# Kernel optimization log

Hardware: AMD Instinct MI355X
Metric: run time of the kernel (lower is better)

## Reference

```python
import jax, jax.numpy as jnp
import numpy as np

D_MODEL = 1024
N_HEADS = 16
HEAD_DIM = 64
N_KV_HEADS = 4
D_FF = 4096
LN_EPS = 1e-5


def setup_inputs() -> dict:
    key = jax.random.key(0)
    ks = jax.random.split(key, 10)
    s = lambda fan_in: 1.0 / np.sqrt(fan_in)
    return {
        "x": jax.random.normal(ks[0], (2, 2048, D_MODEL), dtype=jnp.float32),
        "ln_w": jnp.ones((D_MODEL,), dtype=jnp.float32),
        "ln_b": jnp.zeros((D_MODEL,), dtype=jnp.float32),
        # Linear weights stored as (in, out): y = x @ W
        "wq": jax.random.normal(ks[1], (D_MODEL, N_HEADS * HEAD_DIM), dtype=jnp.float32) * s(D_MODEL),
        "wk": jax.random.normal(ks[2], (D_MODEL, N_KV_HEADS * HEAD_DIM), dtype=jnp.float32) * s(D_MODEL),
        "wv": jax.random.normal(ks[3], (D_MODEL, N_KV_HEADS * HEAD_DIM), dtype=jnp.float32) * s(D_MODEL),
        "wo": jax.random.normal(ks[4], (N_HEADS * HEAD_DIM, D_MODEL), dtype=jnp.float32) * s(N_HEADS * HEAD_DIM),
        "w_gate": jax.random.normal(ks[5], (D_MODEL, D_FF), dtype=jnp.float32) * s(D_MODEL),
        "w_up": jax.random.normal(ks[6], (D_MODEL, D_FF), dtype=jnp.float32) * s(D_MODEL),
        "w_down": jax.random.normal(ks[7], (D_FF, D_MODEL), dtype=jnp.float32) * s(D_FF),
    }


def _layernorm(x, w, b):
    mu = jnp.mean(x, axis=-1, keepdims=True)
    var = jnp.var(x, axis=-1, keepdims=True)
    return (x - mu) * jax.lax.rsqrt(var + LN_EPS) * w + b


def _attention(normed, wq, wk, wv, wo):
    B, S, _ = normed.shape
    h, kh, hd = N_HEADS, N_KV_HEADS, HEAD_DIM
    groups = h // kh
    scale = 1.0 / np.sqrt(hd)
    q = (normed @ wq).reshape(B, S, h, hd).transpose(0, 2, 1, 3)   # [B,h,S,hd]
    k = (normed @ wk).reshape(B, S, kh, hd).transpose(0, 2, 1, 3)  # [B,kh,S,hd]
    v = (normed @ wv).reshape(B, S, kh, hd).transpose(0, 2, 1, 3)
    if groups != 1:
        # matches torch repeat_interleave along head dim
        k = jnp.repeat(k, groups, axis=1)
        v = jnp.repeat(v, groups, axis=1)
    scores = jnp.einsum("bhqd,bhkd->bhqk", q, k) * scale
    causal = jnp.tril(jnp.ones((S, S), dtype=bool))
    scores = jnp.where(causal, scores, -jnp.inf)
    attn = jax.nn.softmax(scores, axis=-1)
    out = jnp.einsum("bhqk,bhkd->bhqd", attn, v)
    out = out.transpose(0, 2, 1, 3).reshape(B, S, h * hd)
    return out @ wo


def _ffn(normed, w_gate, w_up, w_down):
    return (jax.nn.silu(normed @ w_gate) * (normed @ w_up)) @ w_down


def reference(x, ln_w, ln_b, wq, wk, wv, wo, w_gate, w_up, w_down):
    normed = _layernorm(x, ln_w, ln_b)
    attn_out = _attention(normed, wq, wk, wv, wo)
    ffn_out = _ffn(normed, w_gate, w_up, w_down)
    return x + attn_out + ffn_out
```

## Files before the change

### kernel.cpp

```cpp
#include <hip/hip_runtime.h>
#include <cstdint>

typedef __bf16 bf16x8 __attribute__((ext_vector_type(8)));
typedef float f32x4 __attribute__((ext_vector_type(4)));
typedef float f32x16 __attribute__((ext_vector_type(16)));
typedef unsigned short u16;

#define MFMA16(a, b, c) __builtin_amdgcn_mfma_f32_16x16x32_bf16((a), (b), (c), 0, 0, 0)
#define MFMA32(a, b, c) __builtin_amdgcn_mfma_f32_32x32x16_bf16((a), (b), (c), 0, 0, 0)

#define GLLDS(gp, lp) __builtin_amdgcn_global_load_lds( \
    (const __attribute__((address_space(1))) uint32_t*)(gp), \
    (__attribute__((address_space(3))) uint32_t*)(lp), 16, 0, 0)

__device__ __forceinline__ u16 f2bf(float f) {
    union { float f; uint32_t u; } v; v.f = f;
    uint32_t u = v.u;
    u += 0x7FFFu + ((u >> 16) & 1u);
    return (u16)(u >> 16);
}
__device__ __forceinline__ float bf2f(u16 h) {
    union { uint32_t u; float f; } v; v.u = ((uint32_t)h) << 16;
    return v.f;
}

__global__ __launch_bounds__(256) void prep_kernel(
    const float* __restrict__ wq, const float* __restrict__ wk,
    const float* __restrict__ wv, const float* __restrict__ wo,
    const float* __restrict__ wg, const float* __restrict__ wu,
    const float* __restrict__ wd,
    const float* __restrict__ x, const float* __restrict__ ln_w,
    const float* __restrict__ ln_b,
    u16* __restrict__ QKVT, u16* __restrict__ WOT, u16* __restrict__ WGT,
    u16* __restrict__ WUT, u16* __restrict__ WDT, u16* __restrict__ NORMED) {
    const int bid = blockIdx.x;
    const int tid = threadIdx.x;

    if (bid < 14848) {
        const float* in; u16* out; int R, C, gx; int t = bid;
        if (t < 1024)              { in = wq; out = QKVT;                         R = 1024; C = 1024; gx = 32; }
        else if ((t -= 1024) < 256)  { in = wk; out = QKVT + (size_t)1024 * 1024; R = 1024; C = 256;  gx = 8; }
        else if ((t -= 256) < 256)   { in = wv; out = QKVT + (size_t)1280 * 1024; R = 1024; C = 256;  gx = 8; }
        else if ((t -= 256) < 1024)  { in = wo; out = WOT;                        R = 1024; C = 1024; gx = 32; }
        else if ((t -= 1024) < 4096) { in = wg; out = WGT;                        R = 1024; C = 4096; gx = 128; }
        else if ((t -= 4096) < 4096) { in = wu; out = WUT;                        R = 1024; C = 4096; gx = 128; }
        else          { t -= 4096;     in = wd; out = WDT;                        R = 4096; C = 1024; gx = 32; }
        const int bx = t % gx, by = t / gx;
        __shared__ float tile[32][33];
        const int c0 = bx * 32, r0 = by * 32;
        const int tx = tid & 31, ty = tid >> 5;
#pragma unroll
        for (int i = ty; i < 32; i += 8)
            tile[i][tx] = in[(size_t)(r0 + i) * C + c0 + tx];
        __syncthreads();
#pragma unroll
        for (int i = ty; i < 32; i += 8)
            out[(size_t)(c0 + i) * R + r0 + tx] = f2bf(tile[tx][i]);
    } else {
        const int row = bid - 14848;
        float4 v = ((const float4*)(x + (size_t)row * 1024))[tid];
        float s = v.x + v.y + v.z + v.w;
        float s2 = v.x * v.x + v.y * v.y + v.z * v.z + v.w * v.w;
#pragma unroll
        for (int off = 1; off < 64; off <<= 1) {
            s += __shfl_xor(s, off);
            s2 += __shfl_xor(s2, off);
        }
        __shared__ float rs[4], rs2[4];
        const int wv4i = tid >> 6;
        if ((tid & 63) == 0) { rs[wv4i] = s; rs2[wv4i] = s2; }
        __syncthreads();
        s = rs[0] + rs[1] + rs[2] + rs[3];
        s2 = rs2[0] + rs2[1] + rs2[2] + rs2[3];
        float mu = s * (1.0f / 1024.0f);
        float var = s2 * (1.0f / 1024.0f) - mu * mu;
        float inv = rsqrtf(var + 1e-5f);
        float4 wv4 = ((const float4*)ln_w)[tid];
        float4 bv4 = ((const float4*)ln_b)[tid];
        ushort4 o;
        o.x = f2bf((v.x - mu) * inv * wv4.x + bv4.x);
        o.y = f2bf((v.y - mu) * inv * wv4.y + bv4.y);
        o.z = f2bf((v.z - mu) * inv * wv4.z + bv4.z);
        o.w = f2bf((v.w - mu) * inv * wv4.w + bv4.w);
        *(ushort4*)(NORMED + (size_t)row * 1024 + tid * 4) = o;
    }
}

__global__ __launch_bounds__(256) void transpose_v(const u16* __restrict__ in, u16* __restrict__ out,
                                                   int in_stride) {
    __shared__ u16 tile[32][33];
    int b = blockIdx.z;
    int c0 = blockIdx.x * 32, s0 = blockIdx.y * 32;
    int tx = threadIdx.x & 31, ty = threadIdx.x >> 5;
#pragma unroll
    for (int i = ty; i < 32; i += 8)
        tile[i][tx] = in[(size_t)(b * 2048 + s0 + i) * in_stride + c0 + tx];
    __syncthreads();
#pragma unroll
    for (int i = ty; i < 32; i += 8)
        out[(size_t)b * 256 * 2048 + (size_t)(c0 + i) * 2048 + s0 + tx] = tile[tx][i];
}

__global__ __launch_bounds__(256) void gemm_bt64(const u16* __restrict__ A, const u16* __restrict__ Bt,
                                                 void* __restrict__ Cv,
                                                 int N, int K, int mode) {
    __shared__ __align__(16) u16 As[128 * 64];
    __shared__ __align__(16) u16 Bs[64 * 64];
    const int tid = threadIdx.x, lane = tid & 63, wv = tid >> 6;
    const int row0 = blockIdx.x * 128, col0 = blockIdx.y * 64;
    const int wr = (wv >> 1) * 64, wc = (wv & 1) * 32;
    const int fr = lane & 15, fg = lane >> 4;
    const int lr8 = lane >> 3;
    const int lc8s = ((lane & 7) ^ lr8) * 8;

    f32x4 acc[4][2];
#pragma unroll
    for (int i = 0; i < 4; ++i)
#pragma unroll
        for (int j = 0; j < 2; ++j) acc[i][j] = (f32x4){0.f, 0.f, 0.f, 0.f};

    const u16* ga = A + (size_t)(row0 + 32 * wv + lr8) * K + lc8s;
    const u16* gb = Bt + (size_t)(col0 + 16 * wv + lr8) * K + lc8s;
    u16* la = As + wv * 2048;
    u16* lb = Bs + wv * 1024;
    const int f7 = fr & 7;

    for (int k0 = 0; k0 < K; k0 += 64) {
        __syncthreads();
        GLLDS(ga + k0, la);
        GLLDS(ga + (size_t)8 * K + k0, la + 512);
        GLLDS(ga + (size_t)16 * K + k0, la + 1024);
        GLLDS(ga + (size_t)24 * K + k0, la + 1536);
        GLLDS(gb + k0, lb);
        GLLDS(gb + (size_t)8 * K + k0, lb + 512);
        __syncthreads();
#pragma unroll
        for (int kk = 0; kk < 2; ++kk) {
            bf16x8 af[4], bfr[2];
#pragma unroll
            for (int i = 0; i < 4; ++i)
                af[i] = *(const bf16x8*)(As + (wr + i * 16 + fr) * 64 + (((kk * 4 + fg) ^ f7) * 8));
#pragma unroll
            for (int j = 0; j < 2; ++j)
                bfr[j] = *(const bf16x8*)(Bs + (wc + j * 16 + fr) * 64 + (((kk * 4 + fg) ^ f7) * 8));
#pragma unroll
            for (int i = 0; i < 4; ++i)
#pragma unroll
                for (int j = 0; j < 2; ++j)
                    acc[i][j] = MFMA16(af[i], bfr[j], acc[i][j]);
        }
    }

    if (mode == 0) {
        u16* C = (u16*)Cv;
#pragma unroll
        for (int i = 0; i < 4; ++i)
#pragma unroll
            for (int j = 0; j < 2; ++j)
#pragma unroll
                for (int r = 0; r < 4; ++r) {
                    int row = row0 + wr + i * 16 + fg * 4 + r;
                    int col = col0 + wc + j * 16 + fr;
                    C[(size_t)row * N + col] = f2bf(acc[i][j][r]);
                }
    } else {
        float* C = (float*)Cv;
#pragma unroll
        for (int i = 0; i < 4; ++i)
#pragma unroll
            for (int j = 0; j < 2; ++j)
#pragma unroll
                for (int r = 0; r < 4; ++r) {
                    int row = row0 + wr + i * 16 + fg * 4 + r;
                    int col = col0 + wc + j * 16 + fr;
                    C[(size_t)row * N + col] = acc[i][j][r];
                }
    }
}

__global__ __launch_bounds__(256) void gemm_out_fused(const u16* __restrict__ A1,
                                                      const u16* __restrict__ B1t,
                                                      const u16* __restrict__ A2,
                                                      const u16* __restrict__ B2t,
                                                      const float* __restrict__ xres,
                                                      float* __restrict__ C) {
    __shared__ __align__(16) u16 As[128 * 64];
    __shared__ __align__(16) u16 Bs[64 * 64];
    const int tid = threadIdx.x, lane = tid & 63, wv = tid >> 6;
    const int row0 = blockIdx.x * 128, col0 = blockIdx.y * 64;
    const int wr = (wv >> 1) * 64, wc = (wv & 1) * 32;
    const int fr = lane & 15, fg = lane >> 4;
    const int lr8 = lane >> 3;
    const int lc8s = ((lane & 7) ^ lr8) * 8;
    const int f7 = fr & 7;

    f32x4 acc[4][2];
#pragma unroll
    for (int i = 0; i < 4; ++i)
#pragma unroll
        for (int j = 0; j < 2; ++j) acc[i][j] = (f32x4){0.f, 0.f, 0.f, 0.f};

    const int rowA = row0 + 32 * wv + lr8;
    const int rowB = col0 + 16 * wv + lr8;
    u16* la = As + wv * 2048;
    u16* lb = Bs + wv * 1024;

    for (int t = 0; t < 80; ++t) {
        const u16* ga;
        const u16* gb;
        size_t sa, sb;
        if (t < 16) {
            const int ko = t * 64;
            ga = A1 + (size_t)rowA * 1024 + ko + lc8s; sa = 1024;
            gb = B1t + (size_t)rowB * 1024 + ko + lc8s; sb = 1024;
        } else {
            const int ko = (t - 16) * 64;
            ga = A2 + (size_t)rowA * 4096 + ko + lc8s; sa = 4096;
            gb = B2t + (size_t)rowB * 4096 + ko + lc8s; sb = 4096;
        }
        __syncthreads();
        GLLDS(ga, la);
        GLLDS(ga + 8 * sa, la + 512);
        GLLDS(ga + 16 * sa, la + 1024);
        GLLDS(ga + 24 * sa, la + 1536);
        GLLDS(gb, lb);
        GLLDS(gb + 8 * sb, lb + 512);
        __syncthreads();
#pragma unroll
        for (int kk = 0; kk < 2; ++kk) {
            bf16x8 af[4], bfr[2];
#pragma unroll
            for (int i = 0; i < 4; ++i)
                af[i] = *(const bf16x8*)(As + (wr + i * 16 + fr) * 64 + (((kk * 4 + fg) ^ f7) * 8));
#pragma unroll
            for (int j = 0; j < 2; ++j)
                bfr[j] = *(const bf16x8*)(Bs + (wc + j * 16 + fr) * 64 + (((kk * 4 + fg) ^ f7) * 8));
#pragma unroll
            for (int i = 0; i < 4; ++i)
#pragma unroll
                for (int j = 0; j < 2; ++j)
                    acc[i][j] = MFMA16(af[i], bfr[j], acc[i][j]);
        }
    }

#pragma unroll
    for (int i = 0; i < 4; ++i)
#pragma unroll
        for (int j = 0; j < 2; ++j)
#pragma unroll
            for (int r = 0; r < 4; ++r) {
                int row = row0 + wr + i * 16 + fg * 4 + r;
                int col = col0 + wc + j * 16 + fr;
                size_t off = (size_t)row * 1024 + col;
                C[off] = acc[i][j][r] + xres[off];
            }
}

__global__ __launch_bounds__(256) void gemm_gateup(const u16* __restrict__ A,
                                                   const u16* __restrict__ Bg,
                                                   const u16* __restrict__ Bu,
                                                   u16* __restrict__ H, int N, int K) {
    __shared__ __align__(16) u16 As[128 * 64];
    __shared__ __align__(16) u16 Bgs[64 * 64];
    __shared__ __align__(16) u16 Bus[64 * 64];
    const int tid = threadIdx.x, lane = tid & 63, wv = tid >> 6;
    const int row0 = blockIdx.x * 128, col0 = blockIdx.y * 64;
    const int wr = (wv >> 1) * 64, wc = (wv & 1) * 32;
    const int fr = lane & 15, fg = lane >> 4;
    const int lr8 = lane >> 3;
    const int lc8s = ((lane & 7) ^ lr8) * 8;

    f32x4 ag[4][2], au[4][2];
#pragma unroll
    for (int i = 0; i < 4; ++i)
#pragma unroll
        for (int j = 0; j < 2; ++j) {
            ag[i][j] = (f32x4){0.f, 0.f, 0.f, 0.f};
            au[i][j] = (f32x4){0.f, 0.f, 0.f, 0.f};
        }

    const u16* ga = A + (size_t)(row0 + 32 * wv + lr8) * K + lc8s;
    const u16* gg = Bg + (size_t)(col0 + 16 * wv + lr8) * K + lc8s;
    const u16* gu = Bu + (size_t)(col0 + 16 * wv + lr8) * K + lc8s;
    u16* la = As + wv * 2048;
    u16* lg = Bgs + wv * 1024;
    u16* lu = Bus + wv * 1024;
    const int f7 = fr & 7;

    for (int k0 = 0; k0 < K; k0 += 64) {
        __syncthreads();
        GLLDS(ga + k0, la);
        GLLDS(ga + (size_t)8 * K + k0, la + 512);
        GLLDS(ga + (size_t)16 * K + k0, la + 1024);
        GLLDS(ga + (size_t)24 * K + k0, la + 1536);
        GLLDS(gg + k0, lg);
        GLLDS(gg + (size_t)8 * K + k0, lg + 512);
        GLLDS(gu + k0, lu);
        GLLDS(gu + (size_t)8 * K + k0, lu + 512);
        __syncthreads();
#pragma unroll
        for (int kk = 0; kk < 2; ++kk) {
            bf16x8 af[4], bg[2], bu[2];
#pragma unroll
            for (int i = 0; i < 4; ++i)
                af[i] = *(const bf16x8*)(As + (wr + i * 16 + fr) * 64 + (((kk * 4 + fg) ^ f7) * 8));
#pragma unroll
            for (int j = 0; j < 2; ++j) {
                bg[j] = *(const bf16x8*)(Bgs + (wc + j * 16 + fr) * 64 + (((kk * 4 + fg) ^ f7) * 8));
                bu[j] = *(const bf16x8*)(Bus + (wc + j * 16 + fr) * 64 + (((kk * 4 + fg) ^ f7) * 8));
            }
#pragma unroll
            for (int i = 0; i < 4; ++i)
#pragma unroll
                for (int j = 0; j < 2; ++j) {
                    ag[i][j] = MFMA16(af[i], bg[j], ag[i][j]);
                    au[i][j] = MFMA16(af[i], bu[j], au[i][j]);
                }
        }
    }

#pragma unroll
    for (int i = 0; i < 4; ++i)
#pragma unroll
        for (int j = 0; j < 2; ++j)
#pragma unroll
            for (int r = 0; r < 4; ++r) {
                int row = row0 + wr + i * 16 + fg * 4 + r;
                int col = col0 + wc + j * 16 + fr;
                float g = ag[i][j][r];
                float sg = g / (1.0f + __expf(-g));
                H[(size_t)row * N + col] = f2bf(sg * au[i][j][r]);
            }
}

__global__ __launch_bounds__(512) void attn_kernel(const u16* __restrict__ qkv,
                                                   const u16* __restrict__ Vt,
                                                   u16* __restrict__ Ob) {
    __shared__ __align__(16) u16 Ks[2][64 * 64];
    __shared__ __align__(16) u16 Vs[2][64 * 64];
    const int tid = threadIdx.x, lane = tid & 63, w = tid >> 6;
    const int bid = blockIdx.x;
    const int qblk = 7 - (bid & 7);
    const int h = (bid >> 3) & 15;
    const int b = bid >> 7;
    const int kh = h >> 2;
    const int q0 = qblk * 256;
    const int lo = lane & 31, hi = lane >> 5;
    const int qg = q0 + w * 32 + lo;
    const int S = 2048, QS = 1536;

    bf16x8 qf[4];
    {
        const u16* qrow = qkv + (size_t)(b * S + qg) * QS + h * 64 + 8 * hi;
        qf[0] = *(const bf16x8*)(qrow);
        qf[1] = *(const bf16x8*)(qrow + 16);
        qf[2] = *(const bf16x8*)(qrow + 32);
        qf[3] = *(const bf16x8*)(qrow + 48);
    }

    f32x16 o0 = {}, o1 = {};
    float mr = -1e30f, ls = 0.f;
    const int nt = (q0 >> 6) + 4;
    const int wq0 = q0 + w * 32;

    const int sr = w * 8 + (lane >> 3);
    const int scb = ((lane & 7) ^ (sr & 7)) * 8;
    const u16* kg = qkv + (size_t)b * S * QS + 1024 + kh * 64 + scb;
    const u16* vg = Vt + (size_t)(b * 4 + kh) * 64 * 2048 + (size_t)sr * 2048 + scb;
    u16* lk = (u16*)Ks + w * 512;
    u16* lv = (u16*)Vs + w * 512;

#define STAGE(buf, t) { const int kv0s = (t) * 64; \
    GLLDS(kg + (size_t)(kv0s + sr) * QS, lk + (buf) * 4096); \
    GLLDS(vg + kv0s, lv + (buf) * 4096); }

    STAGE(0, 0)
    asm volatile("s_waitcnt vmcnt(0)" ::: "memory");
    __syncthreads();

    const int lrow = lo * 64;
    const int l7 = lo & 7;

    for (int t = 0; t < nt; ++t) {
        const int cur = t & 1;
        if (t + 1 < nt) STAGE(cur ^ 1, t + 1)
        const int kv0 = t * 64;
        if (kv0 <= wq0 + 31) {
            const u16* KB = (const u16*)Ks + cur * 4096;
            const u16* VB = (const u16*)Vs + cur * 4096;
            f32x16 sc0 = {}, sc1 = {};
#pragma unroll
            for (int ds = 0; ds < 4; ++ds) {
                bf16x8 kf0 = *(const bf16x8*)(KB + lrow + (((2 * ds + hi) ^ l7) * 8));
                sc0 = MFMA32(kf0, qf[ds], sc0);
                bf16x8 kf1 = *(const bf16x8*)(KB + 2048 + lrow + (((2 * ds + hi) ^ l7) * 8));
                sc1 = MFMA32(kf1, qf[ds], sc1);
            }

            float xv[32];
            if (kv0 + 63 <= wq0) {
#pragma unroll
                for (int i = 0; i < 16; ++i) {
                    xv[i] = sc0[i] * 0.125f;
                    xv[16 + i] = sc1[i] * 0.125f;
                }
            } else {
#pragma unroll
                for (int i = 0; i < 16; ++i) {
                    int k0g = kv0 + (i & 3) + 8 * (i >> 2) + 4 * hi;
                    xv[i]      = (k0g      <= qg) ? sc0[i] * 0.125f : -1e30f;
                    xv[16 + i] = (k0g + 32 <= qg) ? sc1[i] * 0.125f : -1e30f;
                }
            }
            float m = xv[0];
#pragma unroll
            for (int i = 1; i < 32; ++i) m = fmaxf(m, xv[i]);
            m = fmaxf(m, __shfl_xor(m, 32));
            float nm = fmaxf(mr, m);
            float al = __expf(mr - nm);
            mr = nm;
            float sum = 0.f;
#pragma unroll
            for (int i = 0; i < 32; ++i) {
                float p = __expf(xv[i] - nm);
                xv[i] = p;
                sum += p;
            }
            sum += __shfl_xor(sum, 32);
            ls = ls * al + sum;
#pragma unroll
            for (int i = 0; i < 16; ++i) { o0[i] *= al; o1[i] *= al; }

            bf16x8 pf[4];
#pragma unroll
            for (int g = 0; g < 4; ++g) {
                uint32_t w0, w1, w2, w3;
                asm("v_cvt_pk_bf16_f32 %0, %1, %2" : "=v"(w0) : "v"(xv[g * 8 + 0]), "v"(xv[g * 8 + 1]));
                asm("v_cvt_pk_bf16_f32 %0, %1, %2" : "=v"(w1) : "v"(xv[g * 8 + 2]), "v"(xv[g * 8 + 3]));
                asm("v_cvt_pk_bf16_f32 %0, %1, %2" : "=v"(w2) : "v"(xv[g * 8 + 4]), "v"(xv[g * 8 + 5]));
                asm("v_cvt_pk_bf16_f32 %0, %1, %2" : "=v"(w3) : "v"(xv[g * 8 + 6]), "v"(xv[g * 8 + 7]));
                asm volatile("v_permlane32_swap_b32 %0, %1" : "+v"(w0), "+v"(w2));
                asm volatile("v_permlane32_swap_b32 %0, %1" : "+v"(w1), "+v"(w3));
                union { uint32_t u[4]; bf16x8 v; } pk;
                pk.u[0] = w0; pk.u[1] = w1; pk.u[2] = w2; pk.u[3] = w3;
                pf[g] = pk.v;
            }

#pragma unroll
            for (int ks = 0; ks < 4; ++ks) {
                bf16x8 vf0 = *(const bf16x8*)(VB + lrow + (((2 * ks + hi) ^ l7) * 8));
                o0 = MFMA32(vf0, pf[ks], o0);
                bf16x8 vf1 = *(const bf16x8*)(VB + 2048 + lrow + (((2 * ks + hi) ^ l7) * 8));
                o1 = MFMA32(vf1, pf[ks], o1);
            }
        }
        asm volatile("s_waitcnt vmcnt(0)" ::: "memory");
        __syncthreads();
    }
#undef STAGE

    const float inv = 1.0f / ls;
    u16* orow = Ob + (size_t)(b * S + qg) * 1024 + h * 64;
#pragma unroll
    for (int rg = 0; rg < 4; ++rg) {
        ushort4 w4;
        w4.x = f2bf(o0[rg * 4 + 0] * inv);
        w4.y = f2bf(o0[rg * 4 + 1] * inv);
        w4.z = f2bf(o0[rg * 4 + 2] * inv);
        w4.w = f2bf(o0[rg * 4 + 3] * inv);
        *(ushort4*)(orow + rg * 8 + 4 * hi) = w4;
        w4.x = f2bf(o1[rg * 4 + 0] * inv);
        w4.y = f2bf(o1[rg * 4 + 1] * inv);
        w4.z = f2bf(o1[rg * 4 + 2] * inv);
        w4.w = f2bf(o1[rg * 4 + 3] * inv);
        *(ushort4*)(orow + 32 + rg * 8 + 4 * hi) = w4;
    }
}

extern "C" void kernel_launch(void* const* d_in, const int* in_sizes, int n_in,
                              void* d_out, int out_size, void* d_ws, size_t ws_size,
                              hipStream_t stream) {
    const float* x    = (const float*)d_in[0];
    const float* ln_w = (const float*)d_in[1];
    const float* ln_b = (const float*)d_in[2];
    const float* wq   = (const float*)d_in[3];
    const float* wk   = (const float*)d_in[4];
    const float* wv   = (const float*)d_in[5];
    const float* wo   = (const float*)d_in[6];
    const float* wg   = (const float*)d_in[7];
    const float* wu   = (const float*)d_in[8];
    const float* wd   = (const float*)d_in[9];
    float* out = (float*)d_out;

    char* ws = (char*)d_ws;
    u16* QKVT   = (u16*)(ws + 0x0000000);
    u16* WOT    = (u16*)(ws + 0x0300000);
    u16* WGT    = (u16*)(ws + 0x0500000);
    u16* WUT    = (u16*)(ws + 0x0D00000);
    u16* WDT    = (u16*)(ws + 0x1500000);
    u16* NORMED = (u16*)(ws + 0x1D00000);
    u16* QKV    = (u16*)(ws + 0x2500000);
    u16* VT     = (u16*)(ws + 0x3100000);
    u16* ATTN   = (u16*)(ws + 0x3300000);
    u16* Hb     = (u16*)(ws + 0x3B00000);

    prep_kernel<<<18944, 256, 0, stream>>>(wq, wk, wv, wo, wg, wu, wd,
                                           x, ln_w, ln_b,
                                           QKVT, WOT, WGT, WUT, WDT, NORMED);

    gemm_bt64<<<dim3(32, 24), 256, 0, stream>>>(NORMED, QKVT, QKV, 1536, 1024, 0);
    transpose_v<<<dim3(8, 64, 2), 256, 0, stream>>>(QKV + 1280, VT, 1536);
    attn_kernel<<<256, 512, 0, stream>>>(QKV, VT, ATTN);

    gemm_gateup<<<dim3(32, 64), 256, 0, stream>>>(NORMED, WGT, WUT, Hb, 4096, 1024);

    gemm_out_fused<<<dim3(32, 16), 256, 0, stream>>>(ATTN, WOT, Hb, WDT, x, out);
}
```

Baseline: 252.3 us.

## Merge QKV projection and gate/up GEMM into one heterogeneous launch

Combines the QKV projection GEMM and the gate/up SwiGLU GEMM into a single kernel whose blocks branch on blockIdx: the first 2048 blocks compute gate/up with SiLU, the remaining 768 compute QKV. This removes one launch and lets the small QKV GEMM fill the GPU alongside the larger FFN GEMM instead of running as an under-occupied separate wave. Because the QKV tiles now run after the gate/up blocks in dispatch order, attention starts only after both finish, and the shared-memory footprint of the QKV branch grows to that of the gate/up branch.

```diff
diff --git a/kernel.cpp b/kernel.cpp
--- a/kernel.cpp
+++ b/kernel.cpp
@@ -101,58 +101,74 @@
         out[(size_t)b * 256 * 2048 + (size_t)(c0 + i) * 2048 + s0 + tx] = tile[tx][i];
 }
 
-__global__ __launch_bounds__(256) void gemm_bt64(const u16* __restrict__ A, const u16* __restrict__ Bt,
-                                                 void* __restrict__ Cv,
-                                                 int N, int K, int mode) {
+__global__ __launch_bounds__(256) void gemm_nproj(const u16* __restrict__ A,
+                                                  const u16* __restrict__ Bg,
+                                                  const u16* __restrict__ Bu,
+                                                  const u16* __restrict__ Bqkv,
+                                                  u16* __restrict__ H,
+                                                  u16* __restrict__ QKV) {
     __shared__ __align__(16) u16 As[128 * 64];
     __shared__ __align__(16) u16 Bs[64 * 64];
+    __shared__ __align__(16) u16 Bs2[64 * 64];
     const int tid = threadIdx.x, lane = tid & 63, wv = tid >> 6;
-    const int row0 = blockIdx.x * 128, col0 = blockIdx.y * 64;
     const int wr = (wv >> 1) * 64, wc = (wv & 1) * 32;
     const int fr = lane & 15, fg = lane >> 4;
     const int lr8 = lane >> 3;
     const int lc8s = ((lane & 7) ^ lr8) * 8;
-
-    f32x4 acc[4][2];
-#pragma unroll
-    for (int i = 0; i < 4; ++i)
-#pragma unroll
-        for (int j = 0; j < 2; ++j) acc[i][j] = (f32x4){0.f, 0.f, 0.f, 0.f};
-
-    const u16* ga = A + (size_t)(row0 + 32 * wv + lr8) * K + lc8s;
-    const u16* gb = Bt + (size_t)(col0 + 16 * wv + lr8) * K + lc8s;
-    u16* la = As + wv * 2048;
-    u16* lb = Bs + wv * 1024;
     const int f7 = fr & 7;
-
-    for (int k0 = 0; k0 < K; k0 += 64) {
-        __syncthreads();
-        GLLDS(ga + k0, la);
-        GLLDS(ga + (size_t)8 * K + k0, la + 512);
-        GLLDS(ga + (size_t)16 * K + k0, la + 1024);
-        GLLDS(ga + (size_t)24 * K + k0, la + 1536);
-        GLLDS(gb + k0, lb);
-        GLLDS(gb + (size_t)8 * K + k0, lb + 512);
-        __syncthreads();
-#pragma unroll
-        for (int kk = 0; kk < 2; ++kk) {
-            bf16x8 af[4], bfr[2];
-#pragma unroll
-            for (int i = 0; i < 4; ++i)
-                af[i] = *(const bf16x8*)(As + (wr + i * 16 + fr) * 64 + (((kk * 4 + fg) ^ f7) * 8));
-#pragma unroll
-            for (int j = 0; j < 2; ++j)
-                bfr[j] = *(const bf16x8*)(Bs + (wc + j * 16 + fr) * 64 + (((kk * 4 + fg) ^ f7) * 8));
-#pragma unroll
-            for (int i = 0; i < 4; ++i)
-#pragma unroll
-                for (int j = 0; j < 2; ++j)
-                    acc[i][j] = MFMA16(af[i], bfr[j], acc[i][j]);
-        }
-    }
-
-    if (mode == 0) {
-        u16* C = (u16*)Cv;
+    const int K = 1024;
+
+    if (blockIdx.x < 2048) {
+        const int row0 = (blockIdx.x & 31) * 128, col0 = (blockIdx.x >> 5) * 64;
+
+        f32x4 ag[4][2], au[4][2];
+#pragma unroll
+        for (int i = 0; i < 4; ++i)
+#pragma unroll
+            for (int j = 0; j < 2; ++j) {
+                ag[i][j] = (f32x4){0.f, 0.f, 0.f, 0.f};
+                au[i][j] = (f32x4){0.f, 0.f, 0.f, 0.f};
+            }
+
+        const u16* ga = A + (size_t)(row0 + 32 * wv + lr8) * K + lc8s;
+        const u16* gg = Bg + (size_t)(col0 + 16 * wv + lr8) * K + lc8s;
+        const u16* gu = Bu + (size_t)(col0 + 16 * wv + lr8) * K + lc8s;
+        u16* la = As + wv * 2048;
+        u16* lg = Bs + wv * 1024;
+        u16* lu = Bs2 + wv * 1024;
+
+        for (int k0 = 0; k0 < K; k0 += 64) {
+            __syncthreads();
+            GLLDS(ga + k0, la);
+            GLLDS(ga + (size_t)8 * K + k0, la + 512);
+            GLLDS(ga + (size_t)16 * K + k0, la + 1024);
+            GLLDS(ga + (size_t)24 * K + k0, la + 1536);
+            GLLDS(gg + k0, lg);
+            GLLDS(gg + (size_t)8 * K + k0, lg + 512);
+            GLLDS(gu + k0, lu);
+            GLLDS(gu + (size_t)8 * K + k0, lu + 512);
+            __syncthreads();
+#pragma unroll
+            for (int kk = 0; kk < 2; ++kk) {
+                bf16x8 af[4], bg[2], bu[2];
+#pragma unroll
+                for (int i = 0; i < 4; ++i)
+                    af[i] = *(const bf16x8*)(As + (wr + i * 16 + fr) * 64 + (((kk * 4 + fg) ^ f7) * 8));
+#pragma unroll
+                for (int j = 0; j < 2; ++j) {
+                    bg[j] = *(const bf16x8*)(Bs + (wc + j * 16 + fr) * 64 + (((kk * 4 + fg) ^ f7) * 8));
+                    bu[j] = *(const bf16x8*)(Bs2 + (wc + j * 16 + fr) * 64 + (((kk * 4 + fg) ^ f7) * 8));
+                }
+#pragma unroll
+                for (int i = 0; i < 4; ++i)
+#pragma unroll
+                    for (int j = 0; j < 2; ++j) {
+                        ag[i][j] = MFMA16(af[i], bg[j], ag[i][j]);
+                        au[i][j] = MFMA16(af[i], bu[j], au[i][j]);
+                    }
+            }
+        }
+
 #pragma unroll
         for (int i = 0; i < 4; ++i)
 #pragma unroll
@@ -161,10 +177,51 @@
                 for (int r = 0; r < 4; ++r) {
                     int row = row0 + wr + i * 16 + fg * 4 + r;
                     int col = col0 + wc + j * 16 + fr;
-                    C[(size_t)row * N + col] = f2bf(acc[i][j][r]);
+                    float g = ag[i][j][r];
+                    float sg = g / (1.0f + __expf(-g));
+                    H[(size_t)row * 4096 + col] = f2bf(sg * au[i][j][r]);
                 }
     } else {
-        float* C = (float*)Cv;
+        const int t = blockIdx.x - 2048;
+        const int row0 = (t & 31) * 128, col0 = (t >> 5) * 64;
+
+        f32x4 acc[4][2];
+#pragma unroll
+        for (int i = 0; i < 4; ++i)
+#pragma unroll
+            for (int j = 0; j < 2; ++j) acc[i][j] = (f32x4){0.f, 0.f, 0.f, 0.f};
+
+        const u16* ga = A + (size_t)(row0 + 32 * wv + lr8) * K + lc8s;
+        const u16* gb = Bqkv + (size_t)(col0 + 16 * wv + lr8) * K + lc8s;
+        u16* la = As + wv * 2048;
+        u16* lb = Bs + wv * 1024;
+
+        for (int k0 = 0; k0 < K; k0 += 64) {
+            __syncthreads();
+            GLLDS(ga + k0, la);
+            GLLDS(ga + (size_t)8 * K + k0, la + 512);
+            GLLDS(ga + (size_t)16 * K + k0, la + 1024);
+            GLLDS(ga + (size_t)24 * K + k0, la + 1536);
+            GLLDS(gb + k0, lb);
+            GLLDS(gb + (size_t)8 * K + k0, lb + 512);
+            __syncthreads();
+#pragma unroll
+            for (int kk = 0; kk < 2; ++kk) {
+                bf16x8 af[4], bfr[2];
+#pragma unroll
+                for (int i = 0; i < 4; ++i)
+                    af[i] = *(const bf16x8*)(As + (wr + i * 16 + fr) * 64 + (((kk * 4 + fg) ^ f7) * 8));
+#pragma unroll
+                for (int j = 0; j < 2; ++j)
+                    bfr[j] = *(const bf16x8*)(Bs + (wc + j * 16 + fr) * 64 + (((kk * 4 + fg) ^ f7) * 8));
+#pragma unroll
+                for (int i = 0; i < 4; ++i)
+#pragma unroll
+                    for (int j = 0; j < 2; ++j)
+                        acc[i][j] = MFMA16(af[i], bfr[j], acc[i][j]);
+            }
+        }
+
 #pragma unroll
         for (int i = 0; i < 4; ++i)
 #pragma unroll
@@ -173,7 +230,7 @@
                 for (int r = 0; r < 4; ++r) {
                     int row = row0 + wr + i * 16 + fg * 4 + r;
                     int col = col0 + wc + j * 16 + fr;
-                    C[(size_t)row * N + col] = acc[i][j][r];
+                    QKV[(size_t)row * 1536 + col] = f2bf(acc[i][j][r]);
                 }
     }
 }
@@ -256,83 +313,6 @@
             }
 }
 
-__global__ __launch_bounds__(256) void gemm_gateup(const u16* __restrict__ A,
-                                                   const u16* __restrict__ Bg,
-                                                   const u16* __restrict__ Bu,
-                                                   u16* __restrict__ H, int N, int K) {
-    __shared__ __align__(16) u16 As[128 * 64];
-    __shared__ __align__(16) u16 Bgs[64 * 64];
-    __shared__ __align__(16) u16 Bus[64 * 64];
-    const int tid = threadIdx.x, lane = tid & 63, wv = tid >> 6;
-    const int row0 = blockIdx.x * 128, col0 = blockIdx.y * 64;
-    const int wr = (wv >> 1) * 64, wc = (wv & 1) * 32;
-    const int fr = lane & 15, fg = lane >> 4;
-    const int lr8 = lane >> 3;
-    const int lc8s = ((lane & 7) ^ lr8) * 8;
-
-    f32x4 ag[4][2], au[4][2];
-#pragma unroll
-    for (int i = 0; i < 4; ++i)
-#pragma unroll
-        for (int j = 0; j < 2; ++j) {
-            ag[i][j] = (f32x4){0.f, 0.f, 0.f, 0.f};
-            au[i][j] = (f32x4){0.f, 0.f, 0.f, 0.f};
-        }
-
-    const u16* ga = A + (size_t)(row0 + 32 * wv + lr8) * K + lc8s;
-    const u16* gg = Bg + (size_t)(col0 + 16 * wv + lr8) * K + lc8s;
-    const u16* gu = Bu + (size_t)(col0 + 16 * wv + lr8) * K + lc8s;
-    u16* la = As + wv * 2048;
-    u16* lg = Bgs + wv * 1024;
-    u16* lu = Bus + wv * 1024;
-    const int f7 = fr & 7;
-
-    for (int k0 = 0; k0 < K; k0 += 64) {
-        __syncthreads();
-        GLLDS(ga + k0, la);
-        GLLDS(ga + (size_t)8 * K + k0, la + 512);
-        GLLDS(ga + (size_t)16 * K + k0, la + 1024);
-        GLLDS(ga + (size_t)24 * K + k0, la + 1536);
-        GLLDS(gg + k0, lg);
-        GLLDS(gg + (size_t)8 * K + k0, lg + 512);
-        GLLDS(gu + k0, lu);
-        GLLDS(gu + (size_t)8 * K + k0, lu + 512);
-        __syncthreads();
-#pragma unroll
-        for (int kk = 0; kk < 2; ++kk) {
-            bf16x8 af[4], bg[2], bu[2];
-#pragma unroll
-            for (int i = 0; i < 4; ++i)
-                af[i] = *(const bf16x8*)(As + (wr + i * 16 + fr) * 64 + (((kk * 4 + fg) ^ f7) * 8));
-#pragma unroll
-            for (int j = 0; j < 2; ++j) {
-                bg[j] = *(const bf16x8*)(Bgs + (wc + j * 16 + fr) * 64 + (((kk * 4 + fg) ^ f7) * 8));
-                bu[j] = *(const bf16x8*)(Bus + (wc + j * 16 + fr) * 64 + (((kk * 4 + fg) ^ f7) * 8));
-            }
-#pragma unroll
-            for (int i = 0; i < 4; ++i)
-#pragma unroll
-                for (int j = 0; j < 2; ++j) {
-                    ag[i][j] = MFMA16(af[i], bg[j], ag[i][j]);
-                    au[i][j] = MFMA16(af[i], bu[j], au[i][j]);
-                }
-        }
-    }
-
-#pragma unroll
-    for (int i = 0; i < 4; ++i)
-#pragma unroll
-        for (int j = 0; j < 2; ++j)
-#pragma unroll
-            for (int r = 0; r < 4; ++r) {
-                int row = row0 + wr + i * 16 + fg * 4 + r;
-                int col = col0 + wc + j * 16 + fr;
-                float g = ag[i][j][r];
-                float sg = g / (1.0f + __expf(-g));
-                H[(size_t)row * N + col] = f2bf(sg * au[i][j][r]);
-            }
-}
-
 __global__ __launch_bounds__(512) void attn_kernel(const u16* __restrict__ qkv,
                                                    const u16* __restrict__ Vt,
                                                    u16* __restrict__ Ob) {
@@ -508,11 +488,10 @@
                                            x, ln_w, ln_b,
                                            QKVT, WOT, WGT, WUT, WDT, NORMED);
 
-    gemm_bt64<<<dim3(32, 24), 256, 0, stream>>>(NORMED, QKVT, QKV, 1536, 1024, 0);
+    gemm_nproj<<<2816, 256, 0, stream>>>(NORMED, WGT, WUT, QKVT, Hb, QKV);
+
     transpose_v<<<dim3(8, 64, 2), 256, 0, stream>>>(QKV + 1280, VT, 1536);
     attn_kernel<<<256, 512, 0, stream>>>(QKV, VT, ATTN);
 
-    gemm_gateup<<<dim3(32, 64), 256, 0, stream>>>(NORMED, WGT, WUT, Hb, 4096, 1024);
-
     gemm_out_fused<<<dim3(32, 16), 256, 0, stream>>>(ATTN, WOT, Hb, WDT, x, out);
 }
```

After: 255.5 us. About the same (+1.3%).
